# Performance work log

Measured on AMD Instinct MI355X. Metric: run time of the kernel, lower is better.

## Reference

```python
import jax, jax.numpy as jnp
import numpy as np

N, D, HEADS = 8192, 1024, 8
SCALE = float(np.sqrt(D / HEADS))  # sqrt(dim_head) = sqrt(128)


def setup_inputs() -> dict:
    key = jax.random.key(0)
    ks = jax.random.split(key, 9)
    std = 0.02
    return {
        "x": jax.random.normal(ks[0], (N, D), dtype=jnp.float32),
        "Wq": jax.random.normal(ks[1], (D, D), dtype=jnp.float32) * std,
        "bq": jax.random.normal(ks[2], (D,), dtype=jnp.float32) * std,
        "Wk": jax.random.normal(ks[3], (D, D), dtype=jnp.float32) * std,
        "bk": jax.random.normal(ks[4], (D,), dtype=jnp.float32) * std,
        "Wv": jax.random.normal(ks[5], (D, D), dtype=jnp.float32) * std,
        "bv": jax.random.normal(ks[6], (D,), dtype=jnp.float32) * std,
        "Wo": jax.random.normal(ks[7], (D, D), dtype=jnp.float32) * std,
        "bo": jax.random.normal(ks[8], (D,), dtype=jnp.float32) * std,
    }


def reference(x, Wq, bq, Wk, bk, Wv, bv, Wo, bo):
    # torch nn.Linear: y = x @ W.T + b
    q = x @ Wq.T + bq          # [N, D]
    k = x @ Wk.T + bk          # [N, D]
    v = x @ Wv.T + bv          # [N, D]
    z = q @ k.T                # [N, N]
    att = jax.nn.softmax(z / SCALE, axis=-1)  # softmax over keys (torch dim=1 for 2D)
    out = att @ v              # [N, D]
    out = out @ Wo.T + bo      # output projection
    return out + x             # residual
```

## Files before the change

### kernel.cpp

```cpp
#include <hip/hip_runtime.h>
#include <stdint.h>


#define NTOK 8192
#define DMOD 1024
static constexpr float INV_SCALE = 0.08838834764831845f;

typedef __attribute__((ext_vector_type(8))) short short8;
typedef __attribute__((ext_vector_type(4))) float f32x4;
typedef __attribute__((ext_vector_type(4))) unsigned short u16x4;

__device__ __forceinline__ unsigned short f2bf(float f) {
  union { float f; uint32_t u; } x{f};
  uint32_t r = x.u + 0x7fffu + ((x.u >> 16) & 1u);
  return (unsigned short)(r >> 16);
}
__device__ __forceinline__ void async16(void* lds, const void* g) {
  __builtin_amdgcn_global_load_lds((const __attribute__((address_space(1))) void*)g,
                                   (__attribute__((address_space(3))) void*)lds, 16, 0, 0);
}
__device__ __forceinline__ f32x4 mfma16(short8 a, short8 b, f32x4 c) {
  return __builtin_amdgcn_mfma_f32_16x16x32_bf16(a, b, c, 0, 0, 0);
}

__global__ __launch_bounds__(256) void cast_f32_bf16(const float* __restrict__ in,
                                                     unsigned short* __restrict__ out, int n4) {
  int i = blockIdx.x * 256 + threadIdx.x;
  int stride = gridDim.x * 256;
  for (; i < n4; i += stride) {
    float4 v = ((const float4*)in)[i];
    u16x4 o;
    o[0] = f2bf(v.x); o[1] = f2bf(v.y); o[2] = f2bf(v.z); o[3] = f2bf(v.w);
    ((u16x4*)out)[i] = o;
  }
}

__global__ __launch_bounds__(256) void zerof(float* __restrict__ p, int n) {
  int i = blockIdx.x * 256 + threadIdx.x;
  if (i < n) p[i] = 0.f;
}

template<int BM, int BN, int WM, int WN, bool BIAS, bool TRANS, bool F32OUT, bool RES, bool DIVROW, bool EXPROW>
__global__ __launch_bounds__(WM*WN*64, 2) void gemm_pipe(
    const unsigned short* __restrict__ A, const unsigned short* __restrict__ B,
    unsigned short* __restrict__ O16, float* __restrict__ O32,
    const float* __restrict__ bias, const float* __restrict__ resid,
    float* __restrict__ rowsum,
    int M, int N, int K, float scale)
{
  constexpr int THREADS = WM * WN * 64;
  constexpr int M_REP = BM / (WM * 16);
  constexpr int N_REP = BN / (WN * 16);
  constexpr int ABYTES = BM * 64;
  constexpr int BBYTES = BN * 64;
  constexpr int BUFB = ABYTES + BBYTES;
  constexpr int RPR = THREADS / 4;
  static_assert(BM == BN, "square tiles only");
  static_assert(BM * 64 == RPR * 64 * 2, "2 staging rounds per operand");

  __shared__ alignas(16) char lds[4 * BUFB];

  const int t = threadIdx.x;
  const int l = t & 63, w = t >> 6;
  const int wrow = (w / WN) * (M_REP * 16);
  const int wcol = (w % WN) * (N_REP * 16);

  const int nwg = gridDim.x * gridDim.y;
  const int flat = blockIdx.y * gridDim.x + blockIdx.x;
  const int q8 = nwg >> 3, r8 = nwg & 7;
  const int xcd = flat & 7, pos = flat >> 3;
  const int swz = (xcd < r8 ? xcd * (q8 + 1) : r8 * (q8 + 1) + (xcd - r8) * q8) + pos;
  const int row0 = (swz / gridDim.x) * BM;
  const int col0 = (swz % gridDim.x) * BN;

  const int sr0 = t >> 2, sr1 = (t >> 2) + RPR;
  const int c0 = ((t & 3) ^ ((sr0 >> 1) & 3)) * 8;
  const int c1 = ((t & 3) ^ ((sr1 >> 1) & 3)) * 8;
  const unsigned short* gsrc[4];
  int ldst[4];
  gsrc[0] = A + (size_t)(row0 + sr0) * K + c0;  ldst[0] = t * 16;
  gsrc[1] = A + (size_t)(row0 + sr1) * K + c1;  ldst[1] = t * 16 + RPR * 64;
  gsrc[2] = B + (size_t)(col0 + sr0) * K + c0;  ldst[2] = ABYTES + t * 16;
  gsrc[3] = B + (size_t)(col0 + sr1) * K + c1;  ldst[3] = ABYTES + t * 16 + RPR * 64;

  int offA[M_REP], offB[N_REP];
#pragma unroll
  for (int m = 0; m < M_REP; ++m) {
    int r = wrow + m * 16 + (l & 15);
    offA[m] = r * 64 + (((l >> 4) ^ ((r >> 1) & 3)) * 16);
  }
#pragma unroll
  for (int n = 0; n < N_REP; ++n) {
    int r = wcol + n * 16 + (l & 15);
    offB[n] = ABYTES + r * 64 + (((l >> 4) ^ ((r >> 1) & 3)) * 16);
  }

  f32x4 acc[M_REP][N_REP] = {};
  const int KT = K / 32;

#pragma unroll
  for (int j = 0; j < 3; ++j) {
    char* bb = lds + j * BUFB;
#pragma unroll
    for (int s = 0; s < 4; ++s) async16(bb + ldst[s], gsrc[s] + j * 32);
  }

  for (int t3 = 0; t3 < KT; ++t3) {
    asm volatile("s_waitcnt lgkmcnt(0)" ::: "memory");
    __builtin_amdgcn_s_barrier();
    asm volatile("" ::: "memory");
    if (t3 + 3 < KT) {
      char* bb = lds + ((t3 + 3) & 3) * BUFB;
#pragma unroll
      for (int s = 0; s < 4; ++s) async16(bb + ldst[s], gsrc[s] + (size_t)(t3 + 3) * 32);
      asm volatile("s_waitcnt vmcnt(12)" ::: "memory");
    } else if (t3 + 3 == KT) {
      asm volatile("s_waitcnt vmcnt(8)" ::: "memory");
    } else if (t3 + 2 == KT) {
      asm volatile("s_waitcnt vmcnt(4)" ::: "memory");
    } else {
      asm volatile("s_waitcnt vmcnt(0)" ::: "memory");
    }
    __builtin_amdgcn_s_barrier();
    asm volatile("" ::: "memory");

    const char* bb = lds + (t3 & 3) * BUFB;
    short8 af[M_REP], bf[N_REP];
#pragma unroll
    for (int m = 0; m < M_REP; ++m) af[m] = *(const short8*)(bb + offA[m]);
#pragma unroll
    for (int n = 0; n < N_REP; ++n) bf[n] = *(const short8*)(bb + offB[n]);
#pragma unroll
    for (int m = 0; m < M_REP; ++m)
#pragma unroll
      for (int n = 0; n < N_REP; ++n)
        acc[m][n] = mfma16(af[m], bf[n], acc[m][n]);
  }

  const int rr = (l >> 4) * 4;
  if constexpr (EXPROW) {
#pragma unroll
    for (int m = 0; m < M_REP; ++m) {
#pragma unroll
      for (int j = 0; j < 4; ++j) {
        const int r = row0 + wrow + m * 16 + rr + j;
        float ev[N_REP];
        float part = 0.f;
#pragma unroll
        for (int n = 0; n < N_REP; ++n) { ev[n] = __expf(acc[m][n][j] - 3.0f); part += ev[n]; }
#pragma unroll
        for (int o = 8; o; o >>= 1) part += __shfl_xor(part, o);
        if ((l & 15) == 0) atomicAdd(&rowsum[r], part);
#pragma unroll
        for (int n = 0; n < N_REP; ++n) {
          const int c = col0 + wcol + n * 16 + (l & 15);
          O16[(size_t)r * N + c] = f2bf(ev[n]);
        }
      }
    }
  } else {
#pragma unroll
    for (int m = 0; m < M_REP; ++m) {
#pragma unroll
      for (int n = 0; n < N_REP; ++n) {
#pragma unroll
        for (int j = 0; j < 4; ++j) {
          int r = row0 + wrow + m * 16 + rr + j;
          int c = col0 + wcol + n * 16 + (l & 15);
          float v = acc[m][n][j];
          if (BIAS) v += bias[c];
          v *= scale;
          if (DIVROW) v /= rowsum[r];
          if (RES) v += resid[(size_t)r * N + c];
          if (F32OUT) O32[(size_t)r * N + c] = v;
          else if (TRANS) O16[(size_t)c * M + r] = f2bf(v);
          else O16[(size_t)r * N + c] = f2bf(v);
        }
      }
    }
  }
}

extern "C" void kernel_launch(void* const* d_in, const int* in_sizes, int n_in,
                              void* d_out, int out_size, void* d_ws, size_t ws_size,
                              hipStream_t stream) {
  const float* x  = (const float*)d_in[0];
  const float* Wq = (const float*)d_in[1];
  const float* bq = (const float*)d_in[2];
  const float* Wk = (const float*)d_in[3];
  const float* bk = (const float*)d_in[4];
  const float* Wv = (const float*)d_in[5];
  const float* bv = (const float*)d_in[6];
  const float* Wo = (const float*)d_in[7];
  const float* bo = (const float*)d_in[8];
  float* out = (float*)d_out;

  char* p = (char*)d_ws;
  unsigned short* xb  = (unsigned short*)p; p += (size_t)NTOK * DMOD * 2;
  unsigned short* Wqb = (unsigned short*)p; p += (size_t)DMOD * DMOD * 2;
  unsigned short* Wkb = (unsigned short*)p; p += (size_t)DMOD * DMOD * 2;
  unsigned short* Wvb = (unsigned short*)p; p += (size_t)DMOD * DMOD * 2;
  unsigned short* Wob = (unsigned short*)p; p += (size_t)DMOD * DMOD * 2;
  unsigned short* Qb  = (unsigned short*)p; p += (size_t)NTOK * DMOD * 2;
  unsigned short* Kb  = (unsigned short*)p; p += (size_t)NTOK * DMOD * 2;
  unsigned short* Vt  = (unsigned short*)p; p += (size_t)DMOD * NTOK * 2;
  unsigned short* Ob  = (unsigned short*)p; p += (size_t)NTOK * DMOD * 2;
  float* rowsum       = (float*)p;          p += (size_t)NTOK * 4;
  unsigned short* S   = (unsigned short*)p; p += (size_t)NTOK * NTOK * 2;

  cast_f32_bf16<<<dim3(2048), dim3(256), 0, stream>>>(x, xb, NTOK * DMOD / 4);
  cast_f32_bf16<<<dim3(1024), dim3(256), 0, stream>>>(Wq, Wqb, DMOD * DMOD / 4);
  cast_f32_bf16<<<dim3(1024), dim3(256), 0, stream>>>(Wk, Wkb, DMOD * DMOD / 4);
  cast_f32_bf16<<<dim3(1024), dim3(256), 0, stream>>>(Wv, Wvb, DMOD * DMOD / 4);
  cast_f32_bf16<<<dim3(1024), dim3(256), 0, stream>>>(Wo, Wob, DMOD * DMOD / 4);
  zerof<<<dim3(NTOK / 256), dim3(256), 0, stream>>>(rowsum, NTOK);

  dim3 b512(512), b256(256);
  dim3 gS(NTOK / 256, NTOK / 256);
  dim3 gProj(DMOD / 128, NTOK / 128);

  gemm_pipe<128,128,2,2,true,false,false,false,false,false><<<gProj, b256, 0, stream>>>(xb, Wqb, Qb, nullptr, bq, nullptr, nullptr, NTOK, DMOD, DMOD, INV_SCALE);
  gemm_pipe<128,128,2,2,true,false,false,false,false,false><<<gProj, b256, 0, stream>>>(xb, Wkb, Kb, nullptr, bk, nullptr, nullptr, NTOK, DMOD, DMOD, 1.0f);
  gemm_pipe<128,128,2,2,true,true,false,false,false,false><<<gProj, b256, 0, stream>>>(xb, Wvb, Vt, nullptr, bv, nullptr, nullptr, NTOK, DMOD, DMOD, 1.0f);
  gemm_pipe<256,256,2,4,false,false,false,false,false,true><<<gS, b512, 0, stream>>>(Qb, Kb, S, nullptr, nullptr, nullptr, rowsum, NTOK, NTOK, DMOD, 1.0f);
  gemm_pipe<128,128,2,2,false,false,false,false,true,false><<<gProj, b256, 0, stream>>>(S, Vt, Ob, nullptr, nullptr, nullptr, rowsum, NTOK, DMOD, NTOK, 1.0f);
  gemm_pipe<128,128,2,2,true,false,true,true,false,false><<<gProj, b256, 0, stream>>>(Ob, Wob, nullptr, out, bo, x, nullptr, NTOK, DMOD, DMOD, 1.0f);
}
```

Baseline: 562.4 us.

## Compute softmax row sums via MFMA with ones vector in PV GEMM

Drops the atomic row-sum accumulation in the QK^T epilogue, and with it the zeroing kernel. The PV GEMM now computes each row sum itself with an extra MFMA against a bf16 ones vector and divides in its epilogue. The sums now come from the same bf16-rounded probabilities that are multiplied with V. The PV GEMM also moves to 128x256 tiles with 512 threads, which needed the staging code generalised to non-square tiles. This trades the atomics and the extra launch for extra MFMA work in the large PV GEMM.

```diff
diff --git a/kernel.cpp b/kernel.cpp
--- a/kernel.cpp
+++ b/kernel.cpp
@@ -21,6 +21,16 @@
 }
 __device__ __forceinline__ f32x4 mfma16(short8 a, short8 b, f32x4 c) {
   return __builtin_amdgcn_mfma_f32_16x16x32_bf16(a, b, c, 0, 0, 0);
+}
+template<int N> __device__ __forceinline__ void waitvm() {
+  if constexpr (N == 0)       asm volatile("s_waitcnt vmcnt(0)" ::: "memory");
+  else if constexpr (N == 3)  asm volatile("s_waitcnt vmcnt(3)" ::: "memory");
+  else if constexpr (N == 4)  asm volatile("s_waitcnt vmcnt(4)" ::: "memory");
+  else if constexpr (N == 6)  asm volatile("s_waitcnt vmcnt(6)" ::: "memory");
+  else if constexpr (N == 8)  asm volatile("s_waitcnt vmcnt(8)" ::: "memory");
+  else if constexpr (N == 9)  asm volatile("s_waitcnt vmcnt(9)" ::: "memory");
+  else if constexpr (N == 12) asm volatile("s_waitcnt vmcnt(12)" ::: "memory");
+  else static_assert(N == 0, "unsupported vmcnt");
 }
 
 __global__ __launch_bounds__(256) void cast_f32_bf16(const float* __restrict__ in,
@@ -35,17 +45,11 @@
   }
 }
 
-__global__ __launch_bounds__(256) void zerof(float* __restrict__ p, int n) {
-  int i = blockIdx.x * 256 + threadIdx.x;
-  if (i < n) p[i] = 0.f;
-}
-
-template<int BM, int BN, int WM, int WN, bool BIAS, bool TRANS, bool F32OUT, bool RES, bool DIVROW, bool EXPROW>
+template<int BM, int BN, int WM, int WN, bool BIAS, bool TRANS, bool F32OUT, bool RES, bool EXPO, bool ONES>
 __global__ __launch_bounds__(WM*WN*64, 2) void gemm_pipe(
     const unsigned short* __restrict__ A, const unsigned short* __restrict__ B,
     unsigned short* __restrict__ O16, float* __restrict__ O32,
     const float* __restrict__ bias, const float* __restrict__ resid,
-    float* __restrict__ rowsum,
     int M, int N, int K, float scale)
 {
   constexpr int THREADS = WM * WN * 64;
@@ -54,9 +58,9 @@
   constexpr int ABYTES = BM * 64;
   constexpr int BBYTES = BN * 64;
   constexpr int BUFB = ABYTES + BBYTES;
-  constexpr int RPR = THREADS / 4;
-  static_assert(BM == BN, "square tiles only");
-  static_assert(BM * 64 == RPR * 64 * 2, "2 staging rounds per operand");
+  constexpr int LOADS = BUFB / (THREADS * 16);
+  static_assert(BUFB % (THREADS * 16) == 0, "staging must tile the buffer");
+  static_assert(ABYTES % (THREADS * 16) == 0, "A region aligns to load boundary");
 
   __shared__ alignas(16) char lds[4 * BUFB];
 
@@ -73,15 +77,18 @@
   const int row0 = (swz / gridDim.x) * BM;
   const int col0 = (swz % gridDim.x) * BN;
 
-  const int sr0 = t >> 2, sr1 = (t >> 2) + RPR;
-  const int c0 = ((t & 3) ^ ((sr0 >> 1) & 3)) * 8;
-  const int c1 = ((t & 3) ^ ((sr1 >> 1) & 3)) * 8;
-  const unsigned short* gsrc[4];
-  int ldst[4];
-  gsrc[0] = A + (size_t)(row0 + sr0) * K + c0;  ldst[0] = t * 16;
-  gsrc[1] = A + (size_t)(row0 + sr1) * K + c1;  ldst[1] = t * 16 + RPR * 64;
-  gsrc[2] = B + (size_t)(col0 + sr0) * K + c0;  ldst[2] = ABYTES + t * 16;
-  gsrc[3] = B + (size_t)(col0 + sr1) * K + c1;  ldst[3] = ABYTES + t * 16 + RPR * 64;
+  const unsigned short* gsrc[LOADS];
+  int ldst[LOADS];
+#pragma unroll
+  for (int li = 0; li < LOADS; ++li) {
+    const int byte0 = li * THREADS * 16 + t * 16;
+    int r; const unsigned short* base;
+    if (byte0 < ABYTES) { r = byte0 >> 6; base = A + (size_t)(row0 + r) * K; }
+    else { r = (byte0 - ABYTES) >> 6; base = B + (size_t)(col0 + r) * K; }
+    const int slot = (byte0 >> 4) & 3;
+    gsrc[li] = base + (slot ^ ((r >> 1) & 3)) * 8;
+    ldst[li] = byte0;
+  }
 
   int offA[M_REP], offB[N_REP];
 #pragma unroll
@@ -95,14 +102,19 @@
     offB[n] = ABYTES + r * 64 + (((l >> 4) ^ ((r >> 1) & 3)) * 16);
   }
 
+  short8 bones;
+#pragma unroll
+  for (int i = 0; i < 8; ++i) bones[i] = (short)0x3F80;
+
   f32x4 acc[M_REP][N_REP] = {};
+  f32x4 accrs[M_REP] = {};
   const int KT = K / 32;
 
 #pragma unroll
   for (int j = 0; j < 3; ++j) {
     char* bb = lds + j * BUFB;
 #pragma unroll
-    for (int s = 0; s < 4; ++s) async16(bb + ldst[s], gsrc[s] + j * 32);
+    for (int s = 0; s < LOADS; ++s) async16(bb + ldst[s], gsrc[s] + j * 32);
   }
 
   for (int t3 = 0; t3 < KT; ++t3) {
@@ -112,14 +124,14 @@
     if (t3 + 3 < KT) {
       char* bb = lds + ((t3 + 3) & 3) * BUFB;
 #pragma unroll
-      for (int s = 0; s < 4; ++s) async16(bb + ldst[s], gsrc[s] + (size_t)(t3 + 3) * 32);
-      asm volatile("s_waitcnt vmcnt(12)" ::: "memory");
+      for (int s = 0; s < LOADS; ++s) async16(bb + ldst[s], gsrc[s] + (size_t)(t3 + 3) * 32);
+      waitvm<3 * LOADS>();
     } else if (t3 + 3 == KT) {
-      asm volatile("s_waitcnt vmcnt(8)" ::: "memory");
+      waitvm<2 * LOADS>();
     } else if (t3 + 2 == KT) {
-      asm volatile("s_waitcnt vmcnt(4)" ::: "memory");
+      waitvm<LOADS>();
     } else {
-      asm volatile("s_waitcnt vmcnt(0)" ::: "memory");
+      waitvm<0>();
     }
     __builtin_amdgcn_s_barrier();
     asm volatile("" ::: "memory");
@@ -135,34 +147,42 @@
 #pragma unroll
       for (int n = 0; n < N_REP; ++n)
         acc[m][n] = mfma16(af[m], bf[n], acc[m][n]);
+    if constexpr (ONES) {
+#pragma unroll
+      for (int m = 0; m < M_REP; ++m) accrs[m] = mfma16(af[m], bones, accrs[m]);
+    }
   }
 
   const int rr = (l >> 4) * 4;
-  if constexpr (EXPROW) {
-#pragma unroll
-    for (int m = 0; m < M_REP; ++m) {
+  if constexpr (EXPO) {
+#pragma unroll
+    for (int m = 0; m < M_REP; ++m)
+#pragma unroll
+      for (int n = 0; n < N_REP; ++n)
+#pragma unroll
+        for (int j = 0; j < 4; ++j) {
+          const int r = row0 + wrow + m * 16 + rr + j;
+          const int c = col0 + wcol + n * 16 + (l & 15);
+          O16[(size_t)r * N + c] = f2bf(__expf(acc[m][n][j] - 3.0f));
+        }
+  } else if constexpr (ONES) {
+#pragma unroll
+    for (int m = 0; m < M_REP; ++m)
 #pragma unroll
       for (int j = 0; j < 4; ++j) {
+        const float inv = 1.0f / accrs[m][j];
         const int r = row0 + wrow + m * 16 + rr + j;
-        float ev[N_REP];
-        float part = 0.f;
-#pragma unroll
-        for (int n = 0; n < N_REP; ++n) { ev[n] = __expf(acc[m][n][j] - 3.0f); part += ev[n]; }
-#pragma unroll
-        for (int o = 8; o; o >>= 1) part += __shfl_xor(part, o);
-        if ((l & 15) == 0) atomicAdd(&rowsum[r], part);
 #pragma unroll
         for (int n = 0; n < N_REP; ++n) {
           const int c = col0 + wcol + n * 16 + (l & 15);
-          O16[(size_t)r * N + c] = f2bf(ev[n]);
+          O16[(size_t)r * N + c] = f2bf(acc[m][n][j] * inv);
         }
       }
-    }
   } else {
 #pragma unroll
-    for (int m = 0; m < M_REP; ++m) {
-#pragma unroll
-      for (int n = 0; n < N_REP; ++n) {
+    for (int m = 0; m < M_REP; ++m)
+#pragma unroll
+      for (int n = 0; n < N_REP; ++n)
 #pragma unroll
         for (int j = 0; j < 4; ++j) {
           int r = row0 + wrow + m * 16 + rr + j;
@@ -170,14 +190,11 @@
           float v = acc[m][n][j];
           if (BIAS) v += bias[c];
           v *= scale;
-          if (DIVROW) v /= rowsum[r];
           if (RES) v += resid[(size_t)r * N + c];
           if (F32OUT) O32[(size_t)r * N + c] = v;
           else if (TRANS) O16[(size_t)c * M + r] = f2bf(v);
           else O16[(size_t)r * N + c] = f2bf(v);
         }
-      }
-    }
   }
 }
 
@@ -205,7 +222,6 @@
   unsigned short* Kb  = (unsigned short*)p; p += (size_t)NTOK * DMOD * 2;
   unsigned short* Vt  = (unsigned short*)p; p += (size_t)DMOD * NTOK * 2;
   unsigned short* Ob  = (unsigned short*)p; p += (size_t)NTOK * DMOD * 2;
-  float* rowsum       = (float*)p;          p += (size_t)NTOK * 4;
   unsigned short* S   = (unsigned short*)p; p += (size_t)NTOK * NTOK * 2;
 
   cast_f32_bf16<<<dim3(2048), dim3(256), 0, stream>>>(x, xb, NTOK * DMOD / 4);
@@ -213,16 +229,16 @@
   cast_f32_bf16<<<dim3(1024), dim3(256), 0, stream>>>(Wk, Wkb, DMOD * DMOD / 4);
   cast_f32_bf16<<<dim3(1024), dim3(256), 0, stream>>>(Wv, Wvb, DMOD * DMOD / 4);
   cast_f32_bf16<<<dim3(1024), dim3(256), 0, stream>>>(Wo, Wob, DMOD * DMOD / 4);
-  zerof<<<dim3(NTOK / 256), dim3(256), 0, stream>>>(rowsum, NTOK);
 
   dim3 b512(512), b256(256);
   dim3 gS(NTOK / 256, NTOK / 256);
   dim3 gProj(DMOD / 128, NTOK / 128);
-
-  gemm_pipe<128,128,2,2,true,false,false,false,false,false><<<gProj, b256, 0, stream>>>(xb, Wqb, Qb, nullptr, bq, nullptr, nullptr, NTOK, DMOD, DMOD, INV_SCALE);
-  gemm_pipe<128,128,2,2,true,false,false,false,false,false><<<gProj, b256, 0, stream>>>(xb, Wkb, Kb, nullptr, bk, nullptr, nullptr, NTOK, DMOD, DMOD, 1.0f);
-  gemm_pipe<128,128,2,2,true,true,false,false,false,false><<<gProj, b256, 0, stream>>>(xb, Wvb, Vt, nullptr, bv, nullptr, nullptr, NTOK, DMOD, DMOD, 1.0f);
-  gemm_pipe<256,256,2,4,false,false,false,false,false,true><<<gS, b512, 0, stream>>>(Qb, Kb, S, nullptr, nullptr, nullptr, rowsum, NTOK, NTOK, DMOD, 1.0f);
-  gemm_pipe<128,128,2,2,false,false,false,false,true,false><<<gProj, b256, 0, stream>>>(S, Vt, Ob, nullptr, nullptr, nullptr, rowsum, NTOK, DMOD, NTOK, 1.0f);
-  gemm_pipe<128,128,2,2,true,false,true,true,false,false><<<gProj, b256, 0, stream>>>(Ob, Wob, nullptr, out, bo, x, nullptr, NTOK, DMOD, DMOD, 1.0f);
-}
+  dim3 gPV(DMOD / 256, NTOK / 128);
+
+  gemm_pipe<128,128,2,2,true,false,false,false,false,false><<<gProj, b256, 0, stream>>>(xb, Wqb, Qb, nullptr, bq, nullptr, NTOK, DMOD, DMOD, INV_SCALE);
+  gemm_pipe<128,128,2,2,true,false,false,false,false,false><<<gProj, b256, 0, stream>>>(xb, Wkb, Kb, nullptr, bk, nullptr, NTOK, DMOD, DMOD, 1.0f);
+  gemm_pipe<128,128,2,2,true,true,false,false,false,false><<<gProj, b256, 0, stream>>>(xb, Wvb, Vt, nullptr, bv, nullptr, NTOK, DMOD, DMOD, 1.0f);
+  gemm_pipe<256,256,2,4,false,false,false,false,true,false><<<gS, b512, 0, stream>>>(Qb, Kb, S, nullptr, nullptr, nullptr, NTOK, NTOK, DMOD, 1.0f);
+  gemm_pipe<128,256,2,4,false,false,false,false,false,true><<<gPV, b512, 0, stream>>>(S, Vt, Ob, nullptr, nullptr, nullptr, NTOK, DMOD, NTOK, 1.0f);
+  gemm_pipe<128,128,2,2,true,false,true,true,false,false><<<gProj, b256, 0, stream>>>(Ob, Wob, nullptr, out, bo, x, NTOK, DMOD, DMOD, 1.0f);
+}
```

New measurement: 516.3 us. -8.2%, faster.
